# Kernel optimization log

Measured on AMD Instinct MI355X. Metric: run time of the kernel, lower is better.

Reference implementation:

```python
import jax, jax.numpy as jnp
import numpy as np

D_MODEL = 512
NUM_HEADS = 8
D_K = D_MODEL // NUM_HEADS


def setup_inputs() -> dict:
    key = jax.random.key(0)
    ks = jax.random.split(key, 11)
    B, S = 2, 4096
    s = 1.0 / np.sqrt(D_MODEL)
    inp = {
        "q": jax.random.normal(ks[0], (B, S, D_MODEL), jnp.float32),
        "k": jax.random.normal(ks[1], (B, S, D_MODEL), jnp.float32),
        "v": jax.random.normal(ks[2], (B, S, D_MODEL), jnp.float32),
        "W_q": jax.random.normal(ks[3], (D_MODEL, D_MODEL), jnp.float32) * s,
        "b_q": jnp.zeros((D_MODEL,), jnp.float32),
        "W_k": jax.random.normal(ks[4], (D_MODEL, D_MODEL), jnp.float32) * s,
        "b_k": jnp.zeros((D_MODEL,), jnp.float32),
        "W_v": jax.random.normal(ks[5], (D_MODEL, D_MODEL), jnp.float32) * s,
        "b_v": jnp.zeros((D_MODEL,), jnp.float32),
        "W_o": jax.random.normal(ks[6], (D_MODEL, D_MODEL), jnp.float32) * s,
        "b_o": jnp.zeros((D_MODEL,), jnp.float32),
    }
    return inp


def reference(q, k, v, W_q, b_q, W_k, b_k, W_v, b_v, W_o, b_o):
    B, S, _ = q.shape

    def proj(x, W, b):
        # Linear then split heads: [B,S,D] -> [B,H,S,d_k]
        y = x @ W.T + b
        return y.reshape(B, S, NUM_HEADS, D_K).transpose(0, 2, 1, 3)

    Q = proj(q, W_q, b_q)
    K = proj(k, W_k, b_k)
    V = proj(v, W_v, b_v)
    scores = jnp.einsum("bhsd,bhtd->bhst", Q, K) / jnp.sqrt(jnp.float32(D_K))
    attn = jax.nn.softmax(scores, axis=-1)  # dropout=0.0 -> identity
    ctx = jnp.einsum("bhst,bhtd->bhsd", attn, V)
    ctx = ctx.transpose(0, 2, 1, 3).reshape(B, S, D_MODEL)
    return ctx @ W_o.T + b_o
```

## Files before the change

### kernel.cpp

```cpp
#include <hip/hip_runtime.h>


#define DM   512
#define NH   8
#define DK   64
#define SEQ  4096
#define BATCH 2
#define MROWS (BATCH*SEQ)
#define KVT  128
#define CSC  0.18033688011112042f
#define MBIAS 12.0f

typedef __attribute__((ext_vector_type(4))) float  f32x4;
typedef __attribute__((ext_vector_type(8))) short  s16x8;
typedef __attribute__((ext_vector_type(4))) short  s16x4;
typedef __attribute__((ext_vector_type(4))) unsigned short u16x4;
typedef __attribute__((ext_vector_type(4))) int    i32x4;
typedef __attribute__((ext_vector_type(2))) int    i32x2;

static __device__ __forceinline__ unsigned short f2bf(float f) {
    union { float f; unsigned int u; } a; a.f = f;
    unsigned int r = a.u + 0x7FFFu + ((a.u >> 16) & 1u);
    return (unsigned short)(r >> 16);
}
static __device__ __forceinline__ int cvtpk(float lo, float hi) {
    int r;
    asm("v_cvt_pk_bf16_f32 %0, %1, %2" : "=v"(r) : "v"(lo), "v"(hi));
    return r;
}
static __device__ __forceinline__ float fexp2(float x) {
    float r;
    asm("v_exp_f32 %0, %1" : "=v"(r) : "v"(x));
    return r;
}
static __device__ __forceinline__ void swap32(int &a, int &b) {
    auto t = __builtin_amdgcn_permlane32_swap(a, b, false, false);
    a = t[0]; b = t[1];
}
static __device__ __forceinline__ void swap16(int &a, int &b) {
    auto t = __builtin_amdgcn_permlane16_swap(a, b, false, false);
    a = t[0]; b = t[1];
}

__global__ __launch_bounds__(256)
void convert_w(const float* __restrict__ W0, const float* __restrict__ W1,
               const float* __restrict__ W2, const float* __restrict__ W3,
               unsigned short* __restrict__ O)
{
    const int idx   = blockIdx.x * 256 + threadIdx.x;
    const int which = idx >> 15;
    const int off   = (idx & 32767) * 8;
    const float* W = (which == 0) ? W0 : (which == 1) ? W1 : (which == 2) ? W2 : W3;
    f32x4 a = *(const f32x4*)(W + off);
    f32x4 b = *(const f32x4*)(W + off + 4);
    i32x4 pk;
    pk[0] = cvtpk(a[0], a[1]); pk[1] = cvtpk(a[2], a[3]);
    pk[2] = cvtpk(b[0], b[1]); pk[3] = cvtpk(b[2], b[3]);
    *(i32x4*)(O + (size_t)which * (DM * DM) + off) = pk;
}

__global__ __launch_bounds__(256)
void gemm_proj3(const float* __restrict__ a0, const float* __restrict__ a1,
                const float* __restrict__ a2,
                const unsigned short* __restrict__ Wb,
                const float* __restrict__ b0, const float* __restrict__ b1,
                const float* __restrict__ b2,
                unsigned short* __restrict__ O0, unsigned short* __restrict__ O1,
                unsigned short* __restrict__ O2)
{
    __shared__ short As[2][128 * 40];
    __shared__ short Bs[2][128 * 40];

    const int z = blockIdx.z;
    const float* A   = (z == 0) ? a0 : (z == 1) ? a1 : a2;
    const short* W   = (const short*)Wb + (size_t)z * DM * DM;
    const float* bias= (z == 0) ? b0 : (z == 1) ? b1 : b2;
    unsigned short* O= (z == 0) ? O0 : (z == 1) ? O1 : O2;
    const float oscale = (z == 0) ? CSC : 1.0f;
    const bool  vt = (z == 2);

    const int tid  = threadIdx.x;
    const int lane = tid & 63;
    const int wid  = tid >> 6;
    const int g = lane >> 4, r = lane & 15;
    const int wm = wid >> 1, wn = wid & 1;
    const int brow = blockIdx.x * 128;
    const int bcol = blockIdx.y * 128;

    const float* agp[4]; int alw[4];
    #pragma unroll
    for (int j = 0; j < 4; ++j) {
        int c = tid + 256 * j;
        int row = c >> 3, cc = c & 7;
        agp[j] = A + (size_t)(brow + row) * DM + cc * 4;
        alw[j] = row * 40 + cc * 4;
    }
    const short* wgp[2]; int wlw[2];
    #pragma unroll
    for (int j = 0; j < 2; ++j) {
        int c = tid + 256 * j;
        int row = c >> 2, cc = c & 3;
        wgp[j] = W + (size_t)(bcol + row) * DM + cc * 8;
        wlw[j] = row * 40 + cc * 8;
    }

    f32x4 acc[4][4];
    #pragma unroll
    for (int i = 0; i < 4; ++i)
        #pragma unroll
        for (int j = 0; j < 4; ++j) acc[i][j] = (f32x4)(0.0f);

    f32x4 ar[4]; s16x8 wr[2];
    #pragma unroll
    for (int j = 0; j < 4; ++j) ar[j] = *(const f32x4*)(agp[j]);
    #pragma unroll
    for (int j = 0; j < 2; ++j) wr[j] = *(const s16x8*)(wgp[j]);

    int cur = 0;
    for (int k0 = 0; k0 < DM; k0 += 32) {
        short* as = As[cur];
        short* bs = Bs[cur];
        #pragma unroll
        for (int j = 0; j < 4; ++j) {
            i32x2 pk;
            pk[0] = cvtpk(ar[j][0], ar[j][1]);
            pk[1] = cvtpk(ar[j][2], ar[j][3]);
            *(i32x2*)(&as[alw[j]]) = pk;
        }
        #pragma unroll
        for (int j = 0; j < 2; ++j) *(s16x8*)(&bs[wlw[j]]) = wr[j];
        if (k0 + 32 < DM) {
            #pragma unroll
            for (int j = 0; j < 4; ++j) ar[j] = *(const f32x4*)(agp[j] + k0 + 32);
            #pragma unroll
            for (int j = 0; j < 2; ++j) wr[j] = *(const s16x8*)(wgp[j] + k0 + 32);
        }
        asm volatile("s_waitcnt lgkmcnt(0)\n\ts_barrier" ::: "memory");
        __builtin_amdgcn_sched_barrier(0);

        s16x8 af[4], bfr[4];
        #pragma unroll
        for (int mf = 0; mf < 4; ++mf)
            af[mf] = *(const s16x8*)(&as[(wm * 64 + mf * 16 + r) * 40 + g * 8]);
        #pragma unroll
        for (int nf = 0; nf < 4; ++nf)
            bfr[nf] = *(const s16x8*)(&bs[(wn * 64 + nf * 16 + r) * 40 + g * 8]);
        #pragma unroll
        for (int mf = 0; mf < 4; ++mf)
            #pragma unroll
            for (int nf = 0; nf < 4; ++nf)
                acc[mf][nf] = __builtin_amdgcn_mfma_f32_16x16x32_bf16(
                    af[mf], bfr[nf], acc[mf][nf], 0, 0, 0);
        cur ^= 1;
    }

    const int ncolbase = bcol + wn * 64;
    const int mrowbase = brow + wm * 64;
    #pragma unroll
    for (int mf = 0; mf < 4; ++mf) {
        #pragma unroll
        for (int nf = 0; nf < 4; ++nf) {
            const int ncol = ncolbase + nf * 16 + r;
            const int m0   = mrowbase + mf * 16 + g * 4;
            const float bv = bias[ncol];
            const int h = ncol >> 6, d = ncol & 63;
            if (!vt) {
                #pragma unroll
                for (int i = 0; i < 4; ++i) {
                    int m = m0 + i;
                    int b = m >> 12, s = m & (SEQ - 1);
                    O[((size_t)(b * NH + h) * SEQ + s) * DK + d] =
                        f2bf((acc[mf][nf][i] + bv) * oscale);
                }
            } else {
                const int b = m0 >> 12, s0 = m0 & (SEQ - 1);
                u16x4 pk;
                #pragma unroll
                for (int i = 0; i < 4; ++i) pk[i] = f2bf(acc[mf][nf][i] + bv);
                *(u16x4*)(&O[((size_t)(b * NH + h) * DK + d) * SEQ + s0]) = pk;
            }
        }
    }
}

__global__ __launch_bounds__(256)
void gemm_out(const unsigned short* __restrict__ Ctx,
              const unsigned short* __restrict__ Wb,
              const float* __restrict__ bias,
              float* __restrict__ O)
{
    __shared__ short As[2][64 * 40];
    __shared__ short Bs[2][128 * 40];

    const int tid  = threadIdx.x;
    const int lane = tid & 63;
    const int wid  = tid >> 6;
    const int g = lane >> 4, r = lane & 15;
    const int wm = wid >> 1, wn = wid & 1;
    const int brow = blockIdx.x * 64;
    const int bcol = blockIdx.y * 128;
    const short* W = (const short*)Wb;

    const short* agp; int alw;
    {
        int row = tid >> 2, cc = tid & 3;
        agp = (const short*)Ctx + (size_t)(brow + row) * DM + cc * 8;
        alw = row * 40 + cc * 8;
    }
    const short* wgp[2]; int wlw[2];
    #pragma unroll
    for (int j = 0; j < 2; ++j) {
        int c = tid + 256 * j;
        int row = c >> 2, cc = c & 3;
        wgp[j] = W + (size_t)(bcol + row) * DM + cc * 8;
        wlw[j] = row * 40 + cc * 8;
    }

    f32x4 acc[2][4];
    #pragma unroll
    for (int i = 0; i < 2; ++i)
        #pragma unroll
        for (int j = 0; j < 4; ++j) acc[i][j] = (f32x4)(0.0f);

    s16x8 ar; s16x8 wr[2];
    ar = *(const s16x8*)agp;
    #pragma unroll
    for (int j = 0; j < 2; ++j) wr[j] = *(const s16x8*)(wgp[j]);

    int cur = 0;
    for (int k0 = 0; k0 < DM; k0 += 32) {
        short* as = As[cur];
        short* bs = Bs[cur];
        *(s16x8*)(&as[alw]) = ar;
        #pragma unroll
        for (int j = 0; j < 2; ++j) *(s16x8*)(&bs[wlw[j]]) = wr[j];
        if (k0 + 32 < DM) {
            ar = *(const s16x8*)(agp + k0 + 32);
            #pragma unroll
            for (int j = 0; j < 2; ++j) wr[j] = *(const s16x8*)(wgp[j] + k0 + 32);
        }
        asm volatile("s_waitcnt lgkmcnt(0)\n\ts_barrier" ::: "memory");
        __builtin_amdgcn_sched_barrier(0);

        s16x8 af[2], bfr[4];
        #pragma unroll
        for (int mf = 0; mf < 2; ++mf)
            af[mf] = *(const s16x8*)(&as[(wm * 32 + mf * 16 + r) * 40 + g * 8]);
        #pragma unroll
        for (int nf = 0; nf < 4; ++nf)
            bfr[nf] = *(const s16x8*)(&bs[(wn * 64 + nf * 16 + r) * 40 + g * 8]);
        #pragma unroll
        for (int mf = 0; mf < 2; ++mf)
            #pragma unroll
            for (int nf = 0; nf < 4; ++nf)
                acc[mf][nf] = __builtin_amdgcn_mfma_f32_16x16x32_bf16(
                    af[mf], bfr[nf], acc[mf][nf], 0, 0, 0);
        cur ^= 1;
    }

    const int ncolbase = bcol + wn * 64;
    const int mrowbase = brow + wm * 32;
    #pragma unroll
    for (int mf = 0; mf < 2; ++mf) {
        #pragma unroll
        for (int nf = 0; nf < 4; ++nf) {
            const int ncol = ncolbase + nf * 16 + r;
            const int m0   = mrowbase + mf * 16 + g * 4;
            const float bv = bias[ncol];
            #pragma unroll
            for (int i = 0; i < 4; ++i)
                O[(size_t)(m0 + i) * DM + ncol] = acc[mf][nf][i] + bv;
        }
    }
}

__global__ __launch_bounds__(512, 4)
void attn_kernel(const unsigned short* __restrict__ Qw,
                 const unsigned short* __restrict__ Kw,
                 const unsigned short* __restrict__ Vtw,
                 unsigned short* __restrict__ Ctx)
{
    __shared__ short Kbuf[2][KVT * 64];
    __shared__ short Vbuf[2][64 * KVT];

    const int tid  = threadIdx.x;
    const int lane = tid & 63;
    const int wid  = tid >> 6;
    const int g = lane >> 4, r = lane & 15;

    const int B   = blockIdx.x;
    const int xcd = B & 7;
    const int j   = B >> 3;
    const int bh  = xcd * 2 + (j >> 5);
    const int qt  = j & 31;
    const int q0  = qt * 128 + wid * 16;

    const short* Qp = (const short*)Qw  + (size_t)bh * SEQ * DK;
    const short* Kp = (const short*)Kw  + (size_t)bh * SEQ * DK;
    const short* Vp = (const short*)Vtw + (size_t)bh * DK * SEQ;

    s16x8 qfr[2];
    #pragma unroll
    for (int df = 0; df < 2; ++df)
        qfr[df] = *(const s16x8*)(Qp + (size_t)(q0 + r) * DK + df * 32 + g * 8);

    s16x8 ones;
    #pragma unroll
    for (int i = 0; i < 8; ++i) ones[i] = (short)0x3F80;

    f32x4 o[4];
    #pragma unroll
    for (int df = 0; df < 4; ++df) o[df] = (f32x4)(0.0f);
    f32x4 l_acc = (f32x4)(0.0f);

    int    lwk[2], lwv[2];
    size_t kgo[2], vgo[2];
    #pragma unroll
    for (int jj = 0; jj < 2; ++jj) {
        int c = tid + 512 * jj;
        int krow = c >> 3, kcc = c & 7;
        kgo[jj] = (size_t)krow * DK + kcc * 8;
        lwk[jj] = krow * 64 + ((kcc ^ (krow & 7)) * 8);
        int vrow = c >> 4, vcc = c & 15;
        vgo[jj] = (size_t)vrow * SEQ + vcc * 8;
        lwv[jj] = vrow * KVT + ((vcc ^ (vrow & 15)) * 8);
    }

    s16x8 kr[2], vr[2];
    #pragma unroll
    for (int jj = 0; jj < 2; ++jj) {
        kr[jj] = *(const s16x8*)(Kp + kgo[jj]);
        vr[jj] = *(const s16x8*)(Vp + vgo[jj]);
    }

    int cur = 0;
    for (int t0 = 0; t0 < SEQ; t0 += KVT) {
        short* kb = Kbuf[cur];
        short* vb = Vbuf[cur];
        #pragma unroll
        for (int jj = 0; jj < 2; ++jj) {
            *(s16x8*)(&kb[lwk[jj]]) = kr[jj];
            *(s16x8*)(&vb[lwv[jj]]) = vr[jj];
        }
        if (t0 + KVT < SEQ) {
            #pragma unroll
            for (int jj = 0; jj < 2; ++jj) {
                kr[jj] = *(const s16x8*)(Kp + (size_t)(t0 + KVT) * DK + kgo[jj]);
                vr[jj] = *(const s16x8*)(Vp + vgo[jj] + t0 + KVT);
            }
        }
        asm volatile("s_waitcnt lgkmcnt(0)\n\ts_barrier" ::: "memory");
        __builtin_amdgcn_sched_barrier(0);

        f32x4 s[8];
        #pragma unroll
        for (int tf = 0; tf < 8; ++tf) s[tf] = (f32x4)(-MBIAS);
        __builtin_amdgcn_s_setprio(1);
        #pragma unroll
        for (int tf = 0; tf < 8; ++tf) {
            const short* krow = &kb[(tf * 16 + r) * 64];
            s16x8 ka0 = *(const s16x8*)(krow + ((g ^ (r & 7)) * 8));
            s16x8 ka1 = *(const s16x8*)(krow + (((4 | g) ^ (r & 7)) * 8));
            s[tf] = __builtin_amdgcn_mfma_f32_16x16x32_bf16(ka0, qfr[0], s[tf], 0, 0, 0);
            s[tf] = __builtin_amdgcn_mfma_f32_16x16x32_bf16(ka1, qfr[1], s[tf], 0, 0, 0);
        }
        __builtin_amdgcn_s_setprio(0);

        #pragma unroll
        for (int tf = 0; tf < 8; ++tf) {
            s[tf][0] = fexp2(s[tf][0]);
            s[tf][1] = fexp2(s[tf][1]);
            s[tf][2] = fexp2(s[tf][2]);
            s[tf][3] = fexp2(s[tf][3]);
        }

        s16x8 pb[4];
        #pragma unroll
        for (int h = 0; h < 4; ++h) {
            int A0 = cvtpk(s[2 * h][0],     s[2 * h][1]);
            int A1 = cvtpk(s[2 * h][2],     s[2 * h][3]);
            int A2 = cvtpk(s[2 * h + 1][0], s[2 * h + 1][1]);
            int A3 = cvtpk(s[2 * h + 1][2], s[2 * h + 1][3]);
            swap32(A0, A2); swap16(A0, A2);
            swap32(A1, A3); swap16(A1, A3);
            i32x4 w; w[0] = A0; w[1] = A1; w[2] = A2; w[3] = A3;
            pb[h] = __builtin_bit_cast(s16x8, w);
        }

        __builtin_amdgcn_s_setprio(1);
        #pragma unroll
        for (int h = 0; h < 4; ++h)
            l_acc = __builtin_amdgcn_mfma_f32_16x16x32_bf16(ones, pb[h], l_acc, 0, 0, 0);
        #pragma unroll
        for (int df = 0; df < 4; ++df) {
            const short* vrow = &vb[(df * 16 + r) * KVT];
            #pragma unroll
            for (int h = 0; h < 4; ++h) {
                s16x8 va = *(const s16x8*)(vrow + (((h * 4 + g) ^ r) * 8));
                o[df] = __builtin_amdgcn_mfma_f32_16x16x32_bf16(va, pb[h], o[df], 0, 0, 0);
            }
        }
        __builtin_amdgcn_s_setprio(0);

        cur ^= 1;
    }

    const int b = bh >> 3, h2 = bh & 7;
    {
        const float inv = 1.0f / l_acc[0];
        const int q = q0 + r;
        const size_t rowoff = (size_t)(b * SEQ + q) * DM + h2 * DK;
        #pragma unroll
        for (int df = 0; df < 4; ++df) {
            u16x4 pk;
            #pragma unroll
            for (int i = 0; i < 4; ++i) pk[i] = f2bf(o[df][i] * inv);
            *(u16x4*)(&Ctx[rowoff + df * 16 + g * 4]) = pk;
        }
    }
}

extern "C" void kernel_launch(void* const* d_in, const int* in_sizes, int n_in,
                              void* d_out, int out_size, void* d_ws, size_t ws_size,
                              hipStream_t stream)
{
    const float* q  = (const float*)d_in[0];
    const float* k  = (const float*)d_in[1];
    const float* v  = (const float*)d_in[2];
    const float* Wq = (const float*)d_in[3];
    const float* bq = (const float*)d_in[4];
    const float* Wk = (const float*)d_in[5];
    const float* bk = (const float*)d_in[6];
    const float* Wv = (const float*)d_in[7];
    const float* bv = (const float*)d_in[8];
    const float* Wo = (const float*)d_in[9];
    const float* bo = (const float*)d_in[10];

    const size_t NE = (size_t)MROWS * DM;
    unsigned short* ws  = (unsigned short*)d_ws;
    unsigned short* Qw  = ws;
    unsigned short* Kw  = Qw  + NE;
    unsigned short* Vtw = Kw  + NE;
    unsigned short* Ctx = Vtw + NE;
    unsigned short* Wb  = Ctx + NE;

    convert_w<<<512, 256, 0, stream>>>(Wq, Wk, Wv, Wo, Wb);
    dim3 gg3(MROWS / 128, DM / 128, 3);
    gemm_proj3<<<gg3, 256, 0, stream>>>(q, k, v, Wb, bq, bk, bv, Qw, Kw, Vtw);
    attn_kernel<<<512, 512, 0, stream>>>(Qw, Kw, Vtw, Ctx);
    dim3 ggo(MROWS / 64, DM / 128);
    gemm_out<<<ggo, 256, 0, stream>>>(Ctx, Wb + (size_t)3 * DM * DM, bo, (float*)d_out);
}
```

Measured before the change: 124.1 us.

## Give each attention wave two 16-row query fragments and halve threads per block

The attention kernel now launches 256 threads per block (4 waves), and each wave handles 32 query rows as two 16-row fragments instead of one. Each K and V fragment read from shared memory is reused across both query fragments, which halves LDS reads per MFMA. Each thread now issues four global-to-LDS copies per tile instead of two. The cost is roughly double the accumulator and score registers per wave, and fewer waves per block, which may lower occupancy and latency hiding.

```diff
diff --git a/kernel.cpp b/kernel.cpp
--- a/kernel.cpp
+++ b/kernel.cpp
@@ -274,7 +274,7 @@
     }
 }
 
-__global__ __launch_bounds__(512, 4)
+__global__ __launch_bounds__(256, 2)
 void attn_kernel(const unsigned short* __restrict__ Qw,
                  const unsigned short* __restrict__ Kw,
                  const unsigned short* __restrict__ Vtw,
@@ -293,31 +293,36 @@
     const int j   = B >> 3;
     const int bh  = xcd * 2 + (j >> 5);
     const int qt  = j & 31;
-    const int q0  = qt * 128 + wid * 16;
+    const int q0  = qt * 128 + wid * 32;
 
     const short* Qp = (const short*)Qw  + (size_t)bh * SEQ * DK;
     const short* Kp = (const short*)Kw  + (size_t)bh * SEQ * DK;
     const short* Vp = (const short*)Vtw + (size_t)bh * DK * SEQ;
 
-    s16x8 qfr[2];
-    #pragma unroll
-    for (int df = 0; df < 2; ++df)
-        qfr[df] = *(const s16x8*)(Qp + (size_t)(q0 + r) * DK + df * 32 + g * 8);
+    s16x8 qfr[2][2];
+    #pragma unroll
+    for (int qf = 0; qf < 2; ++qf)
+        #pragma unroll
+        for (int df = 0; df < 2; ++df)
+            qfr[qf][df] = *(const s16x8*)(Qp + (size_t)(q0 + qf * 16 + r) * DK + df * 32 + g * 8);
 
     s16x8 ones;
     #pragma unroll
     for (int i = 0; i < 8; ++i) ones[i] = (short)0x3F80;
 
-    f32x4 o[4];
-    #pragma unroll
-    for (int df = 0; df < 4; ++df) o[df] = (f32x4)(0.0f);
-    f32x4 l_acc = (f32x4)(0.0f);
-
-    int    lwk[2], lwv[2];
-    size_t kgo[2], vgo[2];
-    #pragma unroll
-    for (int jj = 0; jj < 2; ++jj) {
-        int c = tid + 512 * jj;
+    f32x4 o[4][2];
+    #pragma unroll
+    for (int df = 0; df < 4; ++df)
+        #pragma unroll
+        for (int qf = 0; qf < 2; ++qf) o[df][qf] = (f32x4)(0.0f);
+    f32x4 l_acc[2];
+    l_acc[0] = (f32x4)(0.0f); l_acc[1] = (f32x4)(0.0f);
+
+    int    lwk[4], lwv[4];
+    size_t kgo[4], vgo[4];
+    #pragma unroll
+    for (int jj = 0; jj < 4; ++jj) {
+        int c = tid + 256 * jj;
         int krow = c >> 3, kcc = c & 7;
         kgo[jj] = (size_t)krow * DK + kcc * 8;
         lwk[jj] = krow * 64 + ((kcc ^ (krow & 7)) * 8);
@@ -326,9 +331,9 @@
         lwv[jj] = vrow * KVT + ((vcc ^ (vrow & 15)) * 8);
     }
 
-    s16x8 kr[2], vr[2];
-    #pragma unroll
-    for (int jj = 0; jj < 2; ++jj) {
+    s16x8 kr[4], vr[4];
+    #pragma unroll
+    for (int jj = 0; jj < 4; ++jj) {
         kr[jj] = *(const s16x8*)(Kp + kgo[jj]);
         vr[jj] = *(const s16x8*)(Vp + vgo[jj]);
     }
@@ -338,13 +343,13 @@
         short* kb = Kbuf[cur];
         short* vb = Vbuf[cur];
         #pragma unroll
-        for (int jj = 0; jj < 2; ++jj) {
+        for (int jj = 0; jj < 4; ++jj) {
             *(s16x8*)(&kb[lwk[jj]]) = kr[jj];
             *(s16x8*)(&vb[lwv[jj]]) = vr[jj];
         }
         if (t0 + KVT < SEQ) {
             #pragma unroll
-            for (int jj = 0; jj < 2; ++jj) {
+            for (int jj = 0; jj < 4; ++jj) {
                 kr[jj] = *(const s16x8*)(Kp + (size_t)(t0 + KVT) * DK + kgo[jj]);
                 vr[jj] = *(const s16x8*)(Vp + vgo[jj] + t0 + KVT);
             }
@@ -352,52 +357,65 @@
         asm volatile("s_waitcnt lgkmcnt(0)\n\ts_barrier" ::: "memory");
         __builtin_amdgcn_sched_barrier(0);
 
-        f32x4 s[8];
-        #pragma unroll
-        for (int tf = 0; tf < 8; ++tf) s[tf] = (f32x4)(-MBIAS);
+        f32x4 s[8][2];
+        #pragma unroll
+        for (int tf = 0; tf < 8; ++tf)
+            #pragma unroll
+            for (int qf = 0; qf < 2; ++qf) s[tf][qf] = (f32x4)(-MBIAS);
         __builtin_amdgcn_s_setprio(1);
         #pragma unroll
         for (int tf = 0; tf < 8; ++tf) {
             const short* krow = &kb[(tf * 16 + r) * 64];
             s16x8 ka0 = *(const s16x8*)(krow + ((g ^ (r & 7)) * 8));
             s16x8 ka1 = *(const s16x8*)(krow + (((4 | g) ^ (r & 7)) * 8));
-            s[tf] = __builtin_amdgcn_mfma_f32_16x16x32_bf16(ka0, qfr[0], s[tf], 0, 0, 0);
-            s[tf] = __builtin_amdgcn_mfma_f32_16x16x32_bf16(ka1, qfr[1], s[tf], 0, 0, 0);
+            #pragma unroll
+            for (int qf = 0; qf < 2; ++qf) {
+                s[tf][qf] = __builtin_amdgcn_mfma_f32_16x16x32_bf16(ka0, qfr[qf][0], s[tf][qf], 0, 0, 0);
+                s[tf][qf] = __builtin_amdgcn_mfma_f32_16x16x32_bf16(ka1, qfr[qf][1], s[tf][qf], 0, 0, 0);
+            }
         }
         __builtin_amdgcn_s_setprio(0);
 
         #pragma unroll
-        for (int tf = 0; tf < 8; ++tf) {
-            s[tf][0] = fexp2(s[tf][0]);
-            s[tf][1] = fexp2(s[tf][1]);
-            s[tf][2] = fexp2(s[tf][2]);
-            s[tf][3] = fexp2(s[tf][3]);
-        }
-
-        s16x8 pb[4];
-        #pragma unroll
-        for (int h = 0; h < 4; ++h) {
-            int A0 = cvtpk(s[2 * h][0],     s[2 * h][1]);
-            int A1 = cvtpk(s[2 * h][2],     s[2 * h][3]);
-            int A2 = cvtpk(s[2 * h + 1][0], s[2 * h + 1][1]);
-            int A3 = cvtpk(s[2 * h + 1][2], s[2 * h + 1][3]);
-            swap32(A0, A2); swap16(A0, A2);
-            swap32(A1, A3); swap16(A1, A3);
-            i32x4 w; w[0] = A0; w[1] = A1; w[2] = A2; w[3] = A3;
-            pb[h] = __builtin_bit_cast(s16x8, w);
-        }
+        for (int tf = 0; tf < 8; ++tf)
+            #pragma unroll
+            for (int qf = 0; qf < 2; ++qf) {
+                s[tf][qf][0] = fexp2(s[tf][qf][0]);
+                s[tf][qf][1] = fexp2(s[tf][qf][1]);
+                s[tf][qf][2] = fexp2(s[tf][qf][2]);
+                s[tf][qf][3] = fexp2(s[tf][qf][3]);
+            }
+
+        s16x8 pb[2][4];
+        #pragma unroll
+        for (int qf = 0; qf < 2; ++qf)
+            #pragma unroll
+            for (int h = 0; h < 4; ++h) {
+                int A0 = cvtpk(s[2 * h][qf][0],     s[2 * h][qf][1]);
+                int A1 = cvtpk(s[2 * h][qf][2],     s[2 * h][qf][3]);
+                int A2 = cvtpk(s[2 * h + 1][qf][0], s[2 * h + 1][qf][1]);
+                int A3 = cvtpk(s[2 * h + 1][qf][2], s[2 * h + 1][qf][3]);
+                swap32(A0, A2); swap16(A0, A2);
+                swap32(A1, A3); swap16(A1, A3);
+                i32x4 w; w[0] = A0; w[1] = A1; w[2] = A2; w[3] = A3;
+                pb[qf][h] = __builtin_bit_cast(s16x8, w);
+            }
 
         __builtin_amdgcn_s_setprio(1);
         #pragma unroll
-        for (int h = 0; h < 4; ++h)
-            l_acc = __builtin_amdgcn_mfma_f32_16x16x32_bf16(ones, pb[h], l_acc, 0, 0, 0);
+        for (int qf = 0; qf < 2; ++qf)
+            #pragma unroll
+            for (int h = 0; h < 4; ++h)
+                l_acc[qf] = __builtin_amdgcn_mfma_f32_16x16x32_bf16(ones, pb[qf][h], l_acc[qf], 0, 0, 0);
         #pragma unroll
         for (int df = 0; df < 4; ++df) {
             const short* vrow = &vb[(df * 16 + r) * KVT];
             #pragma unroll
             for (int h = 0; h < 4; ++h) {
                 s16x8 va = *(const s16x8*)(vrow + (((h * 4 + g) ^ r) * 8));
-                o[df] = __builtin_amdgcn_mfma_f32_16x16x32_bf16(va, pb[h], o[df], 0, 0, 0);
+                #pragma unroll
+                for (int qf = 0; qf < 2; ++qf)
+                    o[df][qf] = __builtin_amdgcn_mfma_f32_16x16x32_bf16(va, pb[qf][h], o[df][qf], 0, 0, 0);
             }
         }
         __builtin_amdgcn_s_setprio(0);
@@ -406,15 +424,16 @@
     }
 
     const int b = bh >> 3, h2 = bh & 7;
-    {
-        const float inv = 1.0f / l_acc[0];
-        const int q = q0 + r;
+    #pragma unroll
+    for (int qf = 0; qf < 2; ++qf) {
+        const float inv = 1.0f / l_acc[qf][0];
+        const int q = q0 + qf * 16 + r;
         const size_t rowoff = (size_t)(b * SEQ + q) * DM + h2 * DK;
         #pragma unroll
         for (int df = 0; df < 4; ++df) {
             u16x4 pk;
             #pragma unroll
-            for (int i = 0; i < 4; ++i) pk[i] = f2bf(o[df][i] * inv);
+            for (int i = 0; i < 4; ++i) pk[i] = f2bf(o[df][qf][i] * inv);
             *(u16x4*)(&Ctx[rowoff + df * 16 + g * 4]) = pk;
         }
     }
@@ -447,7 +466,7 @@
     convert_w<<<512, 256, 0, stream>>>(Wq, Wk, Wv, Wo, Wb);
     dim3 gg3(MROWS / 128, DM / 128, 3);
     gemm_proj3<<<gg3, 256, 0, stream>>>(q, k, v, Wb, bq, bk, bv, Qw, Kw, Vtw);
-    attn_kernel<<<512, 512, 0, stream>>>(Qw, Kw, Vtw, Ctx);
+    attn_kernel<<<512, 256, 0, stream>>>(Qw, Kw, Vtw, Ctx);
     dim3 ggo(MROWS / 64, DM / 128);
     gemm_out<<<ggo, 256, 0, stream>>>(Ctx, Wb + (size_t)3 * DM * DM, bo, (float*)d_out);
 }
```

Result: no change. 123.1 us (-0.9%).

## Software-pipeline QK^T of next KV tile with exp of current tile

Applied to the files above, without the earlier changes.

Restructures the attention loop so the QK^T MFMAs for the next KV tile are interleaved with the exp2 of the current tile's scores, using two ping-ponged score register sets and a 2x unrolled loop. The aim is to overlap transcendental VALU work with matrix-core work. It adds a second barrier per iteration and doubles score registers, so launch bounds drop from 4 to 2 waves per EU, which lowers occupancy.

```diff
diff --git a/kernel.cpp b/kernel.cpp
--- a/kernel.cpp
+++ b/kernel.cpp
@@ -274,7 +274,7 @@
     }
 }
 
-__global__ __launch_bounds__(512, 4)
+__global__ __launch_bounds__(512, 2)
 void attn_kernel(const unsigned short* __restrict__ Qw,
                  const unsigned short* __restrict__ Kw,
                  const unsigned short* __restrict__ Vtw,
@@ -332,78 +332,108 @@
         kr[jj] = *(const s16x8*)(Kp + kgo[jj]);
         vr[jj] = *(const s16x8*)(Vp + vgo[jj]);
     }
-
-    int cur = 0;
-    for (int t0 = 0; t0 < SEQ; t0 += KVT) {
-        short* kb = Kbuf[cur];
-        short* vb = Vbuf[cur];
-        #pragma unroll
-        for (int jj = 0; jj < 2; ++jj) {
-            *(s16x8*)(&kb[lwk[jj]]) = kr[jj];
-            *(s16x8*)(&vb[lwv[jj]]) = vr[jj];
-        }
-        if (t0 + KVT < SEQ) {
-            #pragma unroll
-            for (int jj = 0; jj < 2; ++jj) {
-                kr[jj] = *(const s16x8*)(Kp + (size_t)(t0 + KVT) * DK + kgo[jj]);
-                vr[jj] = *(const s16x8*)(Vp + vgo[jj] + t0 + KVT);
-            }
-        }
-        asm volatile("s_waitcnt lgkmcnt(0)\n\ts_barrier" ::: "memory");
-        __builtin_amdgcn_sched_barrier(0);
-
-        f32x4 s[8];
-        #pragma unroll
-        for (int tf = 0; tf < 8; ++tf) s[tf] = (f32x4)(-MBIAS);
-        __builtin_amdgcn_s_setprio(1);
-        #pragma unroll
-        for (int tf = 0; tf < 8; ++tf) {
-            const short* krow = &kb[(tf * 16 + r) * 64];
-            s16x8 ka0 = *(const s16x8*)(krow + ((g ^ (r & 7)) * 8));
-            s16x8 ka1 = *(const s16x8*)(krow + (((4 | g) ^ (r & 7)) * 8));
-            s[tf] = __builtin_amdgcn_mfma_f32_16x16x32_bf16(ka0, qfr[0], s[tf], 0, 0, 0);
-            s[tf] = __builtin_amdgcn_mfma_f32_16x16x32_bf16(ka1, qfr[1], s[tf], 0, 0, 0);
-        }
-        __builtin_amdgcn_s_setprio(0);
-
-        #pragma unroll
-        for (int tf = 0; tf < 8; ++tf) {
-            s[tf][0] = fexp2(s[tf][0]);
-            s[tf][1] = fexp2(s[tf][1]);
-            s[tf][2] = fexp2(s[tf][2]);
-            s[tf][3] = fexp2(s[tf][3]);
-        }
-
-        s16x8 pb[4];
-        #pragma unroll
-        for (int h = 0; h < 4; ++h) {
-            int A0 = cvtpk(s[2 * h][0],     s[2 * h][1]);
-            int A1 = cvtpk(s[2 * h][2],     s[2 * h][3]);
-            int A2 = cvtpk(s[2 * h + 1][0], s[2 * h + 1][1]);
-            int A3 = cvtpk(s[2 * h + 1][2], s[2 * h + 1][3]);
-            swap32(A0, A2); swap16(A0, A2);
-            swap32(A1, A3); swap16(A1, A3);
-            i32x4 w; w[0] = A0; w[1] = A1; w[2] = A2; w[3] = A3;
-            pb[h] = __builtin_bit_cast(s16x8, w);
-        }
-
-        __builtin_amdgcn_s_setprio(1);
-        #pragma unroll
-        for (int h = 0; h < 4; ++h)
-            l_acc = __builtin_amdgcn_mfma_f32_16x16x32_bf16(ones, pb[h], l_acc, 0, 0, 0);
-        #pragma unroll
-        for (int df = 0; df < 4; ++df) {
-            const short* vrow = &vb[(df * 16 + r) * KVT];
-            #pragma unroll
-            for (int h = 0; h < 4; ++h) {
-                s16x8 va = *(const s16x8*)(vrow + (((h * 4 + g) ^ r) * 8));
-                o[df] = __builtin_amdgcn_mfma_f32_16x16x32_bf16(va, pb[h], o[df], 0, 0, 0);
-            }
-        }
-        __builtin_amdgcn_s_setprio(0);
-
-        cur ^= 1;
-    }
+    #pragma unroll
+    for (int jj = 0; jj < 2; ++jj) {
+        *(s16x8*)(&Kbuf[0][lwk[jj]]) = kr[jj];
+        *(s16x8*)(&Vbuf[0][lwv[jj]]) = vr[jj];
+    }
+    #pragma unroll
+    for (int jj = 0; jj < 2; ++jj) {
+        kr[jj] = *(const s16x8*)(Kp + (size_t)KVT * DK + kgo[jj]);
+        vr[jj] = *(const s16x8*)(Vp + vgo[jj] + KVT);
+    }
+    asm volatile("s_waitcnt lgkmcnt(0)\n\ts_barrier" ::: "memory");
+    __builtin_amdgcn_sched_barrier(0);
+
+    f32x4 sA[8], sB[8];
+    #pragma unroll
+    for (int tf = 0; tf < 8; ++tf) sA[tf] = (f32x4)(-MBIAS);
+    #pragma unroll
+    for (int tf = 0; tf < 8; ++tf) {
+        const short* krow = &Kbuf[0][(tf * 16 + r) * 64];
+        s16x8 ka0 = *(const s16x8*)(krow + ((g ^ (r & 7)) * 8));
+        s16x8 ka1 = *(const s16x8*)(krow + (((4 | g) ^ (r & 7)) * 8));
+        sA[tf] = __builtin_amdgcn_mfma_f32_16x16x32_bf16(ka0, qfr[0], sA[tf], 0, 0, 0);
+        sA[tf] = __builtin_amdgcn_mfma_f32_16x16x32_bf16(ka1, qfr[1], sA[tf], 0, 0, 0);
+    }
+
+#define ATT_BODY(T0, CUR, SCUR, SNXT)                                          \
+  {                                                                            \
+    const bool hasNext = (T0) + KVT < SEQ;                                     \
+    if (hasNext) {                                                             \
+        short* kbw = Kbuf[(CUR) ^ 1];                                          \
+        short* vbw = Vbuf[(CUR) ^ 1];                                          \
+        _Pragma("unroll")                                                      \
+        for (int jj = 0; jj < 2; ++jj) {                                       \
+            *(s16x8*)(&kbw[lwk[jj]]) = kr[jj];                                 \
+            *(s16x8*)(&vbw[lwv[jj]]) = vr[jj];                                 \
+        }                                                                      \
+        if ((T0) + 2 * KVT < SEQ) {                                            \
+            _Pragma("unroll")                                                  \
+            for (int jj = 0; jj < 2; ++jj) {                                   \
+                kr[jj] = *(const s16x8*)(Kp + (size_t)((T0) + 2 * KVT) * DK + kgo[jj]); \
+                vr[jj] = *(const s16x8*)(Vp + vgo[jj] + (T0) + 2 * KVT);       \
+            }                                                                  \
+        }                                                                      \
+    }                                                                          \
+    asm volatile("s_waitcnt lgkmcnt(0)\n\ts_barrier" ::: "memory");            \
+    __builtin_amdgcn_sched_barrier(0);                                         \
+                \
+    _Pragma("unroll")                                                          \
+    for (int tf = 0; tf < 8; ++tf) SNXT[tf] = (f32x4)(-MBIAS);                 \
+    const short* kbN = Kbuf[(CUR) ^ 1];                                        \
+    _Pragma("unroll")                                                          \
+    for (int tf = 0; tf < 8; ++tf) {                                           \
+        SCUR[tf][0] = fexp2(SCUR[tf][0]);                                      \
+        SCUR[tf][1] = fexp2(SCUR[tf][1]);                                      \
+        SCUR[tf][2] = fexp2(SCUR[tf][2]);                                      \
+        SCUR[tf][3] = fexp2(SCUR[tf][3]);                                      \
+        if (hasNext) {                                                         \
+            const short* krow = &kbN[(tf * 16 + r) * 64];                      \
+            s16x8 ka0 = *(const s16x8*)(krow + ((g ^ (r & 7)) * 8));           \
+            s16x8 ka1 = *(const s16x8*)(krow + (((4 | g) ^ (r & 7)) * 8));     \
+            SNXT[tf] = __builtin_amdgcn_mfma_f32_16x16x32_bf16(ka0, qfr[0], SNXT[tf], 0, 0, 0); \
+            SNXT[tf] = __builtin_amdgcn_mfma_f32_16x16x32_bf16(ka1, qfr[1], SNXT[tf], 0, 0, 0); \
+        }                                                                      \
+    }                                                                          \
+                                                                  \
+    s16x8 pb[4];                                                               \
+    _Pragma("unroll")                                                          \
+    for (int h = 0; h < 4; ++h) {                                              \
+        int A0 = cvtpk(SCUR[2 * h][0],     SCUR[2 * h][1]);                    \
+        int A1 = cvtpk(SCUR[2 * h][2],     SCUR[2 * h][3]);                    \
+        int A2 = cvtpk(SCUR[2 * h + 1][0], SCUR[2 * h + 1][1]);                \
+        int A3 = cvtpk(SCUR[2 * h + 1][2], SCUR[2 * h + 1][3]);                \
+        swap32(A0, A2); swap16(A0, A2);                                        \
+        swap32(A1, A3); swap16(A1, A3);                                        \
+        i32x4 w; w[0] = A0; w[1] = A1; w[2] = A2; w[3] = A3;                   \
+        pb[h] = __builtin_bit_cast(s16x8, w);                                  \
+    }                                                                          \
+                                                             \
+    const short* vbC = Vbuf[CUR];                                              \
+    __builtin_amdgcn_s_setprio(1);                                             \
+    _Pragma("unroll")                                                          \
+    for (int h = 0; h < 4; ++h)                                                \
+        l_acc = __builtin_amdgcn_mfma_f32_16x16x32_bf16(ones, pb[h], l_acc, 0, 0, 0); \
+    _Pragma("unroll")                                                          \
+    for (int df = 0; df < 4; ++df) {                                           \
+        const short* vrow = &vbC[(df * 16 + r) * KVT];                         \
+        _Pragma("unroll")                                                      \
+        for (int h = 0; h < 4; ++h) {                                          \
+            s16x8 va = *(const s16x8*)(vrow + (((h * 4 + g) ^ r) * 8));        \
+            o[df] = __builtin_amdgcn_mfma_f32_16x16x32_bf16(va, pb[h], o[df], 0, 0, 0); \
+        }                                                                      \
+    }                                                                          \
+    __builtin_amdgcn_s_setprio(0);                                             \
+    asm volatile("s_waitcnt lgkmcnt(0)\n\ts_barrier" ::: "memory");            \
+    __builtin_amdgcn_sched_barrier(0);                                         \
+  }
+
+    for (int t0 = 0; t0 < SEQ; t0 += 2 * KVT) {
+        ATT_BODY(t0,        0, sA, sB)
+        ATT_BODY(t0 + KVT,  1, sB, sA)
+    }
+#undef ATT_BODY
 
     const int b = bh >> 3, h2 = bh & 7;
     {
```

New measurement: 153.3 us. 1.24x slower.
